# Performance work log

Hardware: AMD Instinct MI355X
Metric: run time of the kernel (lower is better)

## Reference

```python
import jax, jax.numpy as jnp
import numpy as np

B, L, D, IN = 256, 2048, 8, 1
NP = D * (D + 1) // 2
EPS = 1e-4       # finite-difference step in ChristoffelComputer
DIAG_MIN = 0.1   # MetricEncoder diag floor


def setup_inputs() -> dict:
    key = jax.random.key(0)
    ks = jax.random.split(key, 16)
    def w(k, shape, fan_in):
        return jax.random.normal(k, shape, jnp.float32) / np.sqrt(fan_in)
    return {
        'values': jax.random.normal(ks[0], (B, L), jnp.float32),
        'se_in_w': w(ks[1], (2 * D, IN), IN), 'se_in_b': jnp.zeros(2 * D, jnp.float32),
        'se_conv_w': w(ks[2], (D, 2 * D, 3), 2 * D * 3), 'se_conv_b': jnp.zeros(D, jnp.float32),
        'se_out_w': w(ks[3], (D, D), D), 'se_out_b': jnp.zeros(D, jnp.float32),
        'me_w1': w(ks[4], (2 * D, D), D), 'me_b1': jnp.zeros(2 * D, jnp.float32),
        'me_w2': w(ks[5], (NP, 2 * D), 2 * D), 'me_b2': jnp.zeros(NP, jnp.float32),
        'ef_w1': w(ks[6], (2 * D, 2 * D), 2 * D), 'ef_b1': jnp.zeros(2 * D, jnp.float32),
        'ef_w2': w(ks[7], (D, 2 * D), 2 * D), 'ef_b2': jnp.zeros(D, jnp.float32),
        'ef_scale': jnp.asarray(0.1, jnp.float32),
        'mu_w1': w(ks[8], (D, D), D), 'mu_b1': jnp.zeros(D, jnp.float32),
        'mu_w2': w(ks[9], (1, D), D), 'mu_b2': jnp.zeros(1, jnp.float32),
    }


def _linear(x, w, b):
    return x @ w.T + b


def _forward(values, se_in_w, se_in_b, se_conv_w, se_conv_b, se_out_w, se_out_b,
             me_w1, me_b1, me_w2, me_b2, ef_w1, ef_b1, ef_w2, ef_b2, ef_scale,
             mu_w1, mu_b1, mu_w2, mu_b2):
    d = se_out_w.shape[0]
    rows, cols = jnp.tril_indices(d)
    diag = rows == cols

    def metric(zz):
        # MetricEncoder: z -> lower-tri Cholesky L -> g = L @ L^T (SPD)
        p = _linear(jax.nn.silu(_linear(zz, me_w1, me_b1)), me_w2, me_b2)
        vals = jnp.where(diag, jax.nn.softplus(p) + DIAG_MIN, p)
        Lm = jnp.zeros(p.shape[:-1] + (d, d), p.dtype).at[..., rows, cols].set(vals)
        return Lm @ jnp.swapaxes(Lm, -1, -2)

    # StateEncoder: Linear -> Conv1d(k=3, pad=2, keep first L) -> SiLU -> Linear
    x = values[..., None]                                   # [B, L, 1]
    h = _linear(x, se_in_w, se_in_b)                        # [B, L, 2D]
    h = jax.lax.conv_general_dilated(
        jnp.swapaxes(h, 1, 2), se_conv_w, (1,), [(2, 0)],
        dimension_numbers=('NCH', 'OIH', 'NCH')) + se_conv_b[None, :, None]
    z = _linear(jax.nn.silu(jnp.swapaxes(h, 1, 2)), se_out_w, se_out_b)  # [B, L, D]

    g = metric(z)                                           # [B, L, D, D]
    z_last = z[:, -1]                                       # [B, D]
    dz_last = z[:, -1] - z[:, -2]                           # [B, D]

    # ChristoffelComputer (finite differences on the last step only)
    def fd(e):
        return (metric(z_last + EPS * e) - metric(z_last - EPS * e)) / (2 * EPS)
    dg = jnp.moveaxis(jax.vmap(fd)(jnp.eye(d, dtype=z.dtype)), 0, -1)  # [B,a,b,c] = dg_ab/dz_c
    g_inv = jnp.linalg.inv(g[:, -1])                        # [B, D, D]
    # T[l,i,j] = dg[j,l,i] + dg[i,l,j] - dg[i,j,l]
    T = (jnp.transpose(dg, (0, 2, 3, 1)) + jnp.transpose(dg, (0, 2, 1, 3))
         - jnp.transpose(dg, (0, 3, 1, 2)))
    Gamma = 0.5 * jnp.einsum('bkl,blij->bkij', g_inv, T)    # [B, D, D, D]

    # GeodesicAcceleration: a^k = -Gamma^k_ij dz^i dz^j
    a_geo = -jnp.einsum('bkij,bi,bj->bk', Gamma, dz_last, dz_last)

    # ExternalForce
    f_in = jnp.concatenate([z_last, dz_last], axis=-1)
    F_ext = _linear(jnp.tanh(_linear(f_in, ef_w1, ef_b1)), ef_w2, ef_b2) * ef_scale

    d2z = a_geo + F_ext
    mu = _linear(jax.nn.silu(_linear(d2z, mu_w1, mu_b1)), mu_w2, mu_b2)[..., 0]  # [B]
    x_last = values[:, -1]
    dx_last = values[:, -1] - values[:, -2]
    return x_last + dx_last + mu                            # x_new [B]


def reference(values, se_in_w, se_in_b, se_conv_w, se_conv_b, se_out_w, se_out_b,
              me_w1, me_b1, me_w2, me_b2, ef_w1, ef_b1, ef_w2, ef_b2, ef_scale,
              mu_w1, mu_b1, mu_w2, mu_b2):
    return _forward(values, se_in_w, se_in_b, se_conv_w, se_conv_b, se_out_w, se_out_b,
                    me_w1, me_b1, me_w2, me_b2, ef_w1, ef_b1, ef_w2, ef_b2, ef_scale,
                    mu_w1, mu_b1, mu_w2, mu_b2)
```

## Files before the change

### kernel.cpp

```cpp
#include <hip/hip_runtime.h>
#include <math.h>

#define Bn 256
#define Ln 2048
#define EPSd 1e-4
#define DIAG_MIN 0.1

#define W2PAD 17

__device__ __forceinline__ double silu_d(double x) { return x / (1.0 + exp(-x)); }
__device__ __forceinline__ double softplus_d(double x) {
    return fmax(x, 0.0) + log1p(exp(-fabs(x)));
}

__device__ const signed char ROW36[36] = {0,1,1,2,2,2,3,3,3,3,4,4,4,4,4,5,5,5,5,5,5,6,6,6,6,6,6,6,7,7,7,7,7,7,7,7};
__device__ const signed char COL36[36] = {0,0,1,0,1,2,0,1,2,3,0,1,2,3,4,0,1,2,3,4,5,0,1,2,3,4,5,6,0,1,2,3,4,5,6,7};
#define DIAG_MASK ((1ull<<0)|(1ull<<2)|(1ull<<5)|(1ull<<9)|(1ull<<14)|(1ull<<20)|(1ull<<27)|(1ull<<35))

__global__ __launch_bounds__(256) void memodel_kernel(
    const float* __restrict__ values,
    const float* __restrict__ se_in_w, const float* __restrict__ se_in_b,
    const float* __restrict__ se_conv_w, const float* __restrict__ se_conv_b,
    const float* __restrict__ se_out_w, const float* __restrict__ se_out_b,
    const float* __restrict__ me_w1, const float* __restrict__ me_b1,
    const float* __restrict__ me_w2, const float* __restrict__ me_b2,
    const float* __restrict__ ef_w1, const float* __restrict__ ef_b1,
    const float* __restrict__ ef_w2, const float* __restrict__ ef_b2,
    const float* __restrict__ ef_scale,
    const float* __restrict__ mu_w1, const float* __restrict__ mu_b1,
    const float* __restrict__ mu_w2, const float* __restrict__ mu_b2,
    float* __restrict__ out)
{
    const int b = blockIdx.x;
    const int tid = threadIdx.x;

    __shared__ double w_me1[16 * 8], b_me1[16], w_me2[36 * W2PAD], b_me2[36];
    __shared__ double h16[4][16];
    __shared__ double sh[2][8];
    __shared__ double zl[2][8];
    __shared__ double zs[17][8];
    __shared__ double h1s[17][16];
    __shared__ double Lrs[17][36];
    __shared__ double gs[17][36];
    __shared__ double Apart[8][8];
    __shared__ double Bpart[8];
    __shared__ double invdiag[8];
    __shared__ double solveV[8];
    __shared__ double ageo_s[8];
    __shared__ double h2s[16];
    __shared__ double d2z_s[8];
    __shared__ double h3s[8];

    for (int i = tid; i < 128; i += 256) w_me1[i] = (double)me_w1[i];
    for (int i = tid; i < 16;  i += 256) b_me1[i] = (double)me_b1[i];
    for (int i = tid; i < 576; i += 256) {
        int m = i >> 4, j = i & 15;
        w_me2[m * W2PAD + j] = (double)me_w2[i];
    }
    for (int i = tid; i < 36;  i += 256) b_me2[i] = (double)me_b2[i];

    if (tid < 64) {
        int t = tid >> 4, c = tid & 15;
        double v = (double)values[(size_t)b * Ln + (Ln - 4 + t)];
        h16[t][c] = (double)se_in_w[c] * v + (double)se_in_b[c];
    }
    __syncthreads();

    if (tid < 16) {
        int t = tid >> 3, d = tid & 7;
        double s = (double)se_conv_b[d];
        for (int k = 0; k < 3; ++k)
            for (int c = 0; c < 16; ++c)
                s += (double)se_conv_w[d * 48 + c * 3 + k] * h16[t + k][c];
        sh[t][d] = silu_d(s);
    }
    __syncthreads();

    if (tid < 16) {
        int t = tid >> 3, d = tid & 7;
        double s = (double)se_out_b[d];
        for (int c = 0; c < 8; ++c) s += (double)se_out_w[d * 8 + c] * sh[t][c];
        zl[t][d] = s;
    }
    __syncthreads();

    if (tid < 136) {
        int e = tid >> 3, i = tid & 7;
        double v = zl[1][i];
        if (e >= 1 && e <= 8)  { if (i == e - 1) v += EPSd; }
        else if (e >= 9)       { if (i == e - 9) v -= EPSd; }
        zs[e][i] = v;
    }
    __syncthreads();

    for (int idx = tid; idx < 272; idx += 256) {
        int e = idx >> 4, j = idx & 15;
        double s = b_me1[j];
        const double* w = &w_me1[j * 8];
        const double* z = &zs[e][0];
        for (int i = 0; i < 8; ++i) s += w[i] * z[i];
        h1s[e][j] = silu_d(s);
    }
    __syncthreads();

    for (int idx = tid; idx < 612; idx += 256) {
        int e = idx / 36, m = idx - e * 36;
        double s = b_me2[m];
        const double* w = &w_me2[m * W2PAD];
        const double* h = &h1s[e][0];
        for (int j = 0; j < 16; ++j) s += w[j] * h[j];
        if ((DIAG_MASK >> m) & 1ull) s = softplus_d(s) + DIAG_MIN;
        Lrs[e][m] = s;
    }
    __syncthreads();

    for (int idx = tid; idx < 576; idx += 256) {
        int e = 1 + idx / 36, m = idx - (e - 1) * 36;
        int i = ROW36[m], j = COL36[m];
        const double* Li = &Lrs[e][i * (i + 1) / 2];
        const double* Lj = &Lrs[e][j * (j + 1) / 2];
        double s = 0.0;
        for (int k = 0; k <= j; ++k) s += Li[k] * Lj[k];
        gs[e][m] = s;
    }
    __syncthreads();

    if (tid >= 8 && tid < 16) {
        int i = tid - 8;
        invdiag[i] = 1.0 / Lrs[0][i * (i + 1) / 2 + i];
    }
    if (tid < 8) {
        const int r = tid;
        double dz[8];
        for (int i = 0; i < 8; ++i) dz[i] = zl[1][i] - zl[0][i];
        double Dg[8][8];
        const double inv2e = 1.0 / (2.0 * EPSd);
        for (int m = 0; m < 36; ++m) {
            int i = ROW36[m], j = COL36[m];
            double d = (gs[1 + r][m] - gs[9 + r][m]) * inv2e;
            Dg[i][j] = d; Dg[j][i] = d;
        }
        double w[8]; double Br = 0.0;
        for (int l = 0; l < 8; ++l) {
            double s = 0.0;
            for (int i = 0; i < 8; ++i) s += Dg[i][l] * dz[i];
            w[l] = s;
            Br += s * dz[l];
        }
        for (int l = 0; l < 8; ++l) Apart[r][l] = dz[r] * w[l];
        Bpart[r] = Br;
    }
    __syncthreads();

    if (tid < 8) {
        double a = 0.0;
        for (int r = 0; r < 8; ++r) a += Apart[r][tid];
        solveV[tid] = 2.0 * a - Bpart[tid];
    }
    __syncthreads();

    if (tid == 0) {
        double y[8];
        for (int i = 0; i < 8; ++i) {
            double s = solveV[i];
            const double* Li = &Lrs[0][i * (i + 1) / 2];
            for (int j = 0; j < i; ++j) s -= Li[j] * y[j];
            y[i] = s * invdiag[i];
        }
        double x[8];
        for (int i = 7; i >= 0; --i) {
            double s = y[i];
            for (int j = i + 1; j < 8; ++j) s -= Lrs[0][j * (j + 1) / 2 + i] * x[j];
            x[i] = s * invdiag[i];
            ageo_s[i] = -0.5 * x[i];
        }
    }
    __syncthreads();

    if (tid < 16) {
        double s = (double)ef_b1[tid];
        const float* w = &ef_w1[tid * 16];
        for (int i = 0; i < 8; ++i)  s += (double)w[i] * zl[1][i];
        for (int i = 0; i < 8; ++i)  s += (double)w[8 + i] * (zl[1][i] - zl[0][i]);
        h2s[tid] = tanh(s);
    }
    __syncthreads();

    if (tid < 8) {
        double s = (double)ef_b2[tid];
        const float* w = &ef_w2[tid * 16];
        for (int j = 0; j < 16; ++j) s += (double)w[j] * h2s[j];
        d2z_s[tid] = ageo_s[tid] + s * (double)ef_scale[0];
    }
    __syncthreads();

    if (tid < 8) {
        double s = (double)mu_b1[tid];
        const float* w = &mu_w1[tid * 8];
        for (int i = 0; i < 8; ++i) s += (double)w[i] * d2z_s[i];
        h3s[tid] = silu_d(s);
    }
    __syncthreads();

    if (tid == 0) {
        double mu = (double)mu_b2[0];
        for (int j = 0; j < 8; ++j) mu += (double)mu_w2[j] * h3s[j];
        double vL1 = (double)values[(size_t)b * Ln + (Ln - 1)];
        double vL2 = (double)values[(size_t)b * Ln + (Ln - 2)];
        out[b] = (float)(vL1 + (vL1 - vL2) + mu);
    }
}

extern "C" void kernel_launch(void* const* d_in, const int* in_sizes, int n_in,
                              void* d_out, int out_size, void* d_ws, size_t ws_size,
                              hipStream_t stream) {
    (void)in_sizes; (void)n_in; (void)out_size; (void)d_ws; (void)ws_size;
    const float* values    = (const float*)d_in[0];
    const float* se_in_w   = (const float*)d_in[1];
    const float* se_in_b   = (const float*)d_in[2];
    const float* se_conv_w = (const float*)d_in[3];
    const float* se_conv_b = (const float*)d_in[4];
    const float* se_out_w  = (const float*)d_in[5];
    const float* se_out_b  = (const float*)d_in[6];
    const float* me_w1     = (const float*)d_in[7];
    const float* me_b1     = (const float*)d_in[8];
    const float* me_w2     = (const float*)d_in[9];
    const float* me_b2     = (const float*)d_in[10];
    const float* ef_w1     = (const float*)d_in[11];
    const float* ef_b1     = (const float*)d_in[12];
    const float* ef_w2     = (const float*)d_in[13];
    const float* ef_b2     = (const float*)d_in[14];
    const float* ef_scale  = (const float*)d_in[15];
    const float* mu_w1     = (const float*)d_in[16];
    const float* mu_b1     = (const float*)d_in[17];
    const float* mu_w2     = (const float*)d_in[18];
    const float* mu_b2     = (const float*)d_in[19];
    float* out = (float*)d_out;

    hipLaunchKernelGGL(memodel_kernel, dim3(Bn), dim3(256), 0, stream,
                       values, se_in_w, se_in_b, se_conv_w, se_conv_b,
                       se_out_w, se_out_b, me_w1, me_b1, me_w2, me_b2,
                       ef_w1, ef_b1, ef_w2, ef_b2, ef_scale,
                       mu_w1, mu_b1, mu_w2, mu_b2, out);
}
```

Before: 15.93 us.

## Split metric pipeline across waves and drop most block barriers

```diff
diff --git a/kernel.cpp b/kernel.cpp
--- a/kernel.cpp
+++ b/kernel.cpp
@@ -5,7 +5,6 @@
 #define Ln 2048
 #define EPSd 1e-4
 #define DIAG_MIN 0.1
-
 #define W2PAD 17
 
 __device__ __forceinline__ double silu_d(double x) { return x / (1.0 + exp(-x)); }
@@ -33,180 +32,228 @@
 {
     const int b = blockIdx.x;
     const int tid = threadIdx.x;
-
-    __shared__ double w_me1[16 * 8], b_me1[16], w_me2[36 * W2PAD], b_me2[36];
+    const int lane = tid & 63;
+    const int wav = tid >> 6;
+
+    __shared__ float w_me1f[128], b_me1f[16], w_me2f[36 * W2PAD], b_me2f[36];
+    __shared__ float cvwf[384], cvbf[8], sowf[64], sobf[8];
+    __shared__ float ef_w1f[256], ef_b1f[16], ef_w2f[128], ef_b2f[8], ef_sc_f[1];
+    __shared__ float mu_w1f[64], mu_b1f[8], mu_w2f[8], mu_b2f[1];
     __shared__ double h16[4][16];
     __shared__ double sh[2][8];
     __shared__ double zl[2][8];
-    __shared__ double zs[17][8];
     __shared__ double h1s[17][16];
     __shared__ double Lrs[17][36];
     __shared__ double gs[17][36];
-    __shared__ double Apart[8][8];
-    __shared__ double Bpart[8];
-    __shared__ double invdiag[8];
-    __shared__ double solveV[8];
-    __shared__ double ageo_s[8];
-    __shared__ double h2s[16];
-    __shared__ double d2z_s[8];
-    __shared__ double h3s[8];
-
-    for (int i = tid; i < 128; i += 256) w_me1[i] = (double)me_w1[i];
-    for (int i = tid; i < 16;  i += 256) b_me1[i] = (double)me_b1[i];
-    for (int i = tid; i < 576; i += 256) {
-        int m = i >> 4, j = i & 15;
-        w_me2[m * W2PAD + j] = (double)me_w2[i];
-    }
-    for (int i = tid; i < 36;  i += 256) b_me2[i] = (double)me_b2[i];
-
-    if (tid < 64) {
-        int t = tid >> 4, c = tid & 15;
+    __shared__ double Apart[8][8], Bpart[8], invdiag[8], solveV[8];
+    __shared__ double ageo_s[8], h2s[16], d2z_s[8], h3s[8];
+
+    double vL1 = 0.0, vL2 = 0.0;
+
+    if (wav == 0) {
+        const int t = lane >> 4, c = lane & 15;
         double v = (double)values[(size_t)b * Ln + (Ln - 4 + t)];
+        vL1 = (double)values[(size_t)b * Ln + (Ln - 1)];
+        vL2 = (double)values[(size_t)b * Ln + (Ln - 2)];
         h16[t][c] = (double)se_in_w[c] * v + (double)se_in_b[c];
+    } else {
+        const int i0 = tid - 64;
+        for (int i = i0; i < 128; i += 192) w_me1f[i] = me_w1[i];
+        for (int i = i0; i < 16;  i += 192) b_me1f[i] = me_b1[i];
+        for (int i = i0; i < 576; i += 192) w_me2f[(i >> 4) * W2PAD + (i & 15)] = me_w2[i];
+        for (int i = i0; i < 36;  i += 192) b_me2f[i] = me_b2[i];
+        for (int i = i0; i < 384; i += 192) cvwf[i] = se_conv_w[i];
+        for (int i = i0; i < 8;   i += 192) cvbf[i] = se_conv_b[i];
+        for (int i = i0; i < 64;  i += 192) sowf[i] = se_out_w[i];
+        for (int i = i0; i < 8;   i += 192) sobf[i] = se_out_b[i];
+        for (int i = i0; i < 256; i += 192) ef_w1f[i] = ef_w1[i];
+        for (int i = i0; i < 16;  i += 192) ef_b1f[i] = ef_b1[i];
+        for (int i = i0; i < 128; i += 192) ef_w2f[i] = ef_w2[i];
+        for (int i = i0; i < 8;   i += 192) ef_b2f[i] = ef_b2[i];
+        for (int i = i0; i < 64;  i += 192) mu_w1f[i] = mu_w1[i];
+        for (int i = i0; i < 8;   i += 192) mu_b1f[i] = mu_b1[i];
+        for (int i = i0; i < 8;   i += 192) mu_w2f[i] = mu_w2[i];
+        if (i0 == 0) { ef_sc_f[0] = ef_scale[0]; mu_b2f[0] = mu_b2[0]; }
     }
     __syncthreads();
 
-    if (tid < 16) {
-        int t = tid >> 3, d = tid & 7;
-        double s = (double)se_conv_b[d];
-        for (int k = 0; k < 3; ++k)
-            for (int c = 0; c < 16; ++c)
-                s += (double)se_conv_w[d * 48 + c * 3 + k] * h16[t + k][c];
-        sh[t][d] = silu_d(s);
+    if (wav == 0 && lane < 16) {
+        const int tq = lane >> 3, d = lane & 7;
+        {
+            double s = (double)cvbf[d];
+            #pragma unroll
+            for (int k = 0; k < 3; ++k)
+                #pragma unroll
+                for (int c = 0; c < 16; ++c)
+                    s += (double)cvwf[d * 48 + c * 3 + k] * h16[tq + k][c];
+            sh[tq][d] = silu_d(s);
+        }
+        {
+            double s = (double)sobf[d];
+            #pragma unroll
+            for (int c = 0; c < 8; ++c) s += (double)sowf[d * 8 + c] * sh[tq][c];
+            zl[tq][d] = s;
+        }
     }
     __syncthreads();
 
-    if (tid < 16) {
-        int t = tid >> 3, d = tid & 7;
-        double s = (double)se_out_b[d];
-        for (int c = 0; c < 8; ++c) s += (double)se_out_w[d * 8 + c] * sh[t][c];
-        zl[t][d] = s;
+    {
+        const int ebase = 1 + wav * 4;
+        double z1[8];
+        #pragma unroll
+        for (int i = 0; i < 8; ++i) z1[i] = zl[1][i];
+
+        {
+            const int q = lane >> 4, j = lane & 15;
+            const int e = ebase + q;
+            const double sgn = (e <= 8) ? EPSd : -EPSd;
+            const int pid = (e - 1) & 7;
+            double s = (double)b_me1f[j];
+            #pragma unroll
+            for (int i = 0; i < 8; ++i) {
+                double zi = z1[i] + ((i == pid) ? sgn : 0.0);
+                s += (double)w_me1f[j * 8 + i] * zi;
+            }
+            h1s[e][j] = silu_d(s);
+        }
+        if (wav == 3 && lane < 16) {
+            const int j = lane;
+            double s = (double)b_me1f[j];
+            #pragma unroll
+            for (int i = 0; i < 8; ++i) s += (double)w_me1f[j * 8 + i] * z1[i];
+            h1s[0][j] = silu_d(s);
+        }
+
+        #pragma unroll
+        for (int r = 0; r < 3; ++r) {
+            const int idx = lane + r * 64;
+            if (idx < 144) {
+                const int q = idx / 36, m = idx - q * 36;
+                const int e = ebase + q;
+                double s = (double)b_me2f[m];
+                const float* w = &w_me2f[m * W2PAD];
+                const double* h = &h1s[e][0];
+                #pragma unroll
+                for (int j = 0; j < 16; ++j) s += (double)w[j] * h[j];
+                if ((DIAG_MASK >> m) & 1ull) s = softplus_d(s) + DIAG_MIN;
+                Lrs[e][m] = s;
+            }
+        }
+        if (wav == 3 && lane < 36) {
+            const int m = lane;
+            double s = (double)b_me2f[m];
+            const float* w = &w_me2f[m * W2PAD];
+            const double* h = &h1s[0][0];
+            #pragma unroll
+            for (int j = 0; j < 16; ++j) s += (double)w[j] * h[j];
+            if ((DIAG_MASK >> m) & 1ull) s = softplus_d(s) + DIAG_MIN;
+            Lrs[0][m] = s;
+        }
+
+        #pragma unroll
+        for (int r = 0; r < 3; ++r) {
+            const int idx = lane + r * 64;
+            if (idx < 144) {
+                const int q = idx / 36, m = idx - q * 36;
+                const int e = ebase + q;
+                const int i = ROW36[m], j = COL36[m];
+                const double* Li = &Lrs[e][i * (i + 1) / 2];
+                const double* Lj = &Lrs[e][j * (j + 1) / 2];
+                double s = 0.0;
+                for (int k = 0; k <= j; ++k) s += Li[k] * Lj[k];
+                gs[e][m] = s;
+            }
+        }
     }
     __syncthreads();
-
-    if (tid < 136) {
-        int e = tid >> 3, i = tid & 7;
-        double v = zl[1][i];
-        if (e >= 1 && e <= 8)  { if (i == e - 1) v += EPSd; }
-        else if (e >= 9)       { if (i == e - 9) v -= EPSd; }
-        zs[e][i] = v;
-    }
-    __syncthreads();
-
-    for (int idx = tid; idx < 272; idx += 256) {
-        int e = idx >> 4, j = idx & 15;
-        double s = b_me1[j];
-        const double* w = &w_me1[j * 8];
-        const double* z = &zs[e][0];
-        for (int i = 0; i < 8; ++i) s += w[i] * z[i];
-        h1s[e][j] = silu_d(s);
-    }
-    __syncthreads();
-
-    for (int idx = tid; idx < 612; idx += 256) {
-        int e = idx / 36, m = idx - e * 36;
-        double s = b_me2[m];
-        const double* w = &w_me2[m * W2PAD];
-        const double* h = &h1s[e][0];
-        for (int j = 0; j < 16; ++j) s += w[j] * h[j];
-        if ((DIAG_MASK >> m) & 1ull) s = softplus_d(s) + DIAG_MIN;
-        Lrs[e][m] = s;
-    }
-    __syncthreads();
-
-    for (int idx = tid; idx < 576; idx += 256) {
-        int e = 1 + idx / 36, m = idx - (e - 1) * 36;
-        int i = ROW36[m], j = COL36[m];
-        const double* Li = &Lrs[e][i * (i + 1) / 2];
-        const double* Lj = &Lrs[e][j * (j + 1) / 2];
-        double s = 0.0;
-        for (int k = 0; k <= j; ++k) s += Li[k] * Lj[k];
-        gs[e][m] = s;
-    }
-    __syncthreads();
-
-    if (tid >= 8 && tid < 16) {
-        int i = tid - 8;
+    if (wav != 0) return;
+
+    if (lane >= 8 && lane < 16) {
+        const int i = lane - 8;
         invdiag[i] = 1.0 / Lrs[0][i * (i + 1) / 2 + i];
     }
-    if (tid < 8) {
-        const int r = tid;
+    if (lane < 8) {
+        const int r = lane;
         double dz[8];
+        #pragma unroll
         for (int i = 0; i < 8; ++i) dz[i] = zl[1][i] - zl[0][i];
-        double Dg[8][8];
+        double w[8];
+        #pragma unroll
+        for (int l = 0; l < 8; ++l) w[l] = 0.0;
         const double inv2e = 1.0 / (2.0 * EPSd);
+        #pragma unroll
         for (int m = 0; m < 36; ++m) {
-            int i = ROW36[m], j = COL36[m];
+            const int i = ROW36[m], j = COL36[m];
             double d = (gs[1 + r][m] - gs[9 + r][m]) * inv2e;
-            Dg[i][j] = d; Dg[j][i] = d;
-        }
-        double w[8]; double Br = 0.0;
+            w[j] += d * dz[i];
+            if (i != j) w[i] += d * dz[j];
+        }
+        double Br = 0.0;
+        #pragma unroll
         for (int l = 0; l < 8; ++l) {
-            double s = 0.0;
-            for (int i = 0; i < 8; ++i) s += Dg[i][l] * dz[i];
-            w[l] = s;
-            Br += s * dz[l];
-        }
-        for (int l = 0; l < 8; ++l) Apart[r][l] = dz[r] * w[l];
+            Apart[r][l] = dz[r] * w[l];
+            Br += w[l] * dz[l];
+        }
         Bpart[r] = Br;
     }
-    __syncthreads();
-
-    if (tid < 8) {
+
+    if (lane < 8) {
         double a = 0.0;
-        for (int r = 0; r < 8; ++r) a += Apart[r][tid];
-        solveV[tid] = 2.0 * a - Bpart[tid];
-    }
-    __syncthreads();
-
-    if (tid == 0) {
+        #pragma unroll
+        for (int r = 0; r < 8; ++r) a += Apart[r][lane];
+        solveV[lane] = 2.0 * a - Bpart[lane];
+    }
+
+    if (lane == 0) {
         double y[8];
+        #pragma unroll
         for (int i = 0; i < 8; ++i) {
             double s = solveV[i];
-            const double* Li = &Lrs[0][i * (i + 1) / 2];
-            for (int j = 0; j < i; ++j) s -= Li[j] * y[j];
+            #pragma unroll
+            for (int j = 0; j < 8; ++j) if (j < i) s -= Lrs[0][i * (i + 1) / 2 + j] * y[j];
             y[i] = s * invdiag[i];
         }
         double x[8];
+        #pragma unroll
         for (int i = 7; i >= 0; --i) {
             double s = y[i];
-            for (int j = i + 1; j < 8; ++j) s -= Lrs[0][j * (j + 1) / 2 + i] * x[j];
+            #pragma unroll
+            for (int j = 0; j < 8; ++j) if (j > i) s -= Lrs[0][j * (j + 1) / 2 + i] * x[j];
             x[i] = s * invdiag[i];
             ageo_s[i] = -0.5 * x[i];
         }
     }
-    __syncthreads();
-
-    if (tid < 16) {
-        double s = (double)ef_b1[tid];
-        const float* w = &ef_w1[tid * 16];
-        for (int i = 0; i < 8; ++i)  s += (double)w[i] * zl[1][i];
-        for (int i = 0; i < 8; ++i)  s += (double)w[8 + i] * (zl[1][i] - zl[0][i]);
-        h2s[tid] = tanh(s);
-    }
-    __syncthreads();
-
-    if (tid < 8) {
-        double s = (double)ef_b2[tid];
-        const float* w = &ef_w2[tid * 16];
+
+    if (lane < 16) {
+        double s = (double)ef_b1f[lane];
+        const float* w = &ef_w1f[lane * 16];
+        #pragma unroll
+        for (int i = 0; i < 8; ++i) s += (double)w[i] * zl[1][i];
+        #pragma unroll
+        for (int i = 0; i < 8; ++i) s += (double)w[8 + i] * (zl[1][i] - zl[0][i]);
+        h2s[lane] = tanh(s);
+    }
+
+    if (lane < 8) {
+        double s = (double)ef_b2f[lane];
+        const float* w = &ef_w2f[lane * 16];
+        #pragma unroll
         for (int j = 0; j < 16; ++j) s += (double)w[j] * h2s[j];
-        d2z_s[tid] = ageo_s[tid] + s * (double)ef_scale[0];
-    }
-    __syncthreads();
-
-    if (tid < 8) {
-        double s = (double)mu_b1[tid];
-        const float* w = &mu_w1[tid * 8];
+        d2z_s[lane] = ageo_s[lane] + s * (double)ef_sc_f[0];
+    }
+
+    if (lane < 8) {
+        double s = (double)mu_b1f[lane];
+        const float* w = &mu_w1f[lane * 8];
+        #pragma unroll
         for (int i = 0; i < 8; ++i) s += (double)w[i] * d2z_s[i];
-        h3s[tid] = silu_d(s);
-    }
-    __syncthreads();
-
-    if (tid == 0) {
-        double mu = (double)mu_b2[0];
-        for (int j = 0; j < 8; ++j) mu += (double)mu_w2[j] * h3s[j];
-        double vL1 = (double)values[(size_t)b * Ln + (Ln - 1)];
-        double vL2 = (double)values[(size_t)b * Ln + (Ln - 2)];
+        h3s[lane] = silu_d(s);
+    }
+
+    if (lane == 0) {
+        double mu = (double)mu_b2f[0];
+        #pragma unroll
+        for (int j = 0; j < 8; ++j) mu += (double)mu_w2f[j] * h3s[j];
         out[b] = (float)(vL1 + (vL1 - vL2) + mu);
     }
 }
```

New measurement: 17.19 us. +7.9%, slower.
